# Optimization experiments

Measured on AMD Instinct MI355X. Metric: run time of the kernel, lower is better.

The kernel has to match this reference:

```python
import jax, jax.numpy as jnp
import numpy as np

DIM = 1024
NUM_HEADS = 16
HEAD_DIM = DIM // NUM_HEADS


def setup_inputs() -> dict:
    key = jax.random.key(0)
    k_x, k_q, k_k, k_v, k_o = jax.random.split(key, 5)
    B, L = 2, 2048
    scale = 1.0 / np.sqrt(DIM)
    x_bld = jax.random.normal(k_x, (B, L, DIM), dtype=jnp.float32)
    # LinearGeneral kernels: (in_features, num_heads, head_dim) for q/k/v,
    # (num_heads, head_dim, out_features) for out. Init ~ lecun_normal-ish scale.
    Wq = jax.random.normal(k_q, (DIM, NUM_HEADS, HEAD_DIM), dtype=jnp.float32) * scale
    Wk = jax.random.normal(k_k, (DIM, NUM_HEADS, HEAD_DIM), dtype=jnp.float32) * scale
    Wv = jax.random.normal(k_v, (DIM, NUM_HEADS, HEAD_DIM), dtype=jnp.float32) * scale
    Wo = jax.random.normal(k_o, (NUM_HEADS, HEAD_DIM, DIM), dtype=jnp.float32) * scale
    return {"x_bld": x_bld, "Wq": Wq, "Wk": Wk, "Wv": Wv, "Wo": Wo}


def reference(x_bld, Wq, Wk, Wv, Wo) -> jnp.ndarray:
    # Projections: [B,L,D] x [D,H,hd] -> [B,L,H,hd]
    q_blhd = jnp.einsum('bld,dhk->blhk', x_bld, Wq)
    k_blhd = jnp.einsum('bld,dhk->blhk', x_bld, Wk)
    v_blhd = jnp.einsum('bld,dhk->blhk', x_bld, Wv)
    # Scores: [B,H,L,L]
    attn_bhll = jnp.einsum('bqhd,bkhd->bhqk', q_blhd, k_blhd)
    attn_bhll = attn_bhll / jnp.sqrt(jnp.asarray(HEAD_DIM, dtype=attn_bhll.dtype))
    L = x_bld.shape[1]
    qi = jnp.arange(L)[:, None]
    ki = jnp.arange(L)[None, :]
    mask_ll = ki <= qi  # causal, no window
    neg_inf = jnp.finfo(attn_bhll.dtype).min
    attn_bhll = jnp.where(mask_ll[None, None, :, :], attn_bhll, neg_inf)
    attn_bhll = jax.nn.softmax(attn_bhll, axis=-1)
    y_blhd = jnp.einsum('bhqk,bkhd->bqhd', attn_bhll, v_blhd)
    # Output projection: contract (H, hd) -> D
    return jnp.einsum('blhk,hkd->bld', y_blhd, Wo)
```

## Files before the change

kernel.cpp:

```cpp
#include <hip/hip_runtime.h>
#include <hip/hip_bf16.h>

typedef __hip_bfloat16 bf16;
typedef __attribute__((ext_vector_type(8))) short short8;
typedef __attribute__((ext_vector_type(4))) float f32x4;

__device__ __forceinline__ float bfbits2f(unsigned short u) {
    return __uint_as_float(((unsigned int)u) << 16);
}
__device__ __forceinline__ unsigned short f2bfbits(float f) {
    union { float f; unsigned int u; } x;
    x.f = f;
    unsigned int r = x.u + 0x7FFFu + ((x.u >> 16) & 1u);
    return (unsigned short)(r >> 16);
}
__device__ __forceinline__ unsigned int pack_bf16x2(float lo, float hi) {
    unsigned int u0 = __float_as_uint(lo) + 0x8000u;
    unsigned int u1 = __float_as_uint(hi) + 0x8000u;
    return __builtin_amdgcn_perm(u1, u0, 0x07060302u);
}
__device__ __forceinline__ void async_copy16(const void* g, void* l) {
    __builtin_amdgcn_global_load_lds(
        (const __attribute__((address_space(1))) void*)g,
        (__attribute__((address_space(3))) void*)l, 16, 0, 0);
}
__device__ __forceinline__ bool sniff_bf16(const unsigned int* p, int lane) {
    unsigned int wd = p[lane];
    unsigned int e = (wd >> 7) & 0xFFu;
    return __popcll(__ballot(e >= 90u && e <= 150u)) > 40;
}

__global__ __launch_bounds__(256) void prep(
    const void* __restrict__ X, const void* __restrict__ W1,
    const void* __restrict__ W2, const void* __restrict__ W3,
    const void* __restrict__ W4, short* __restrict__ xb,
    short* __restrict__ O1, short* __restrict__ O2,
    short* __restrict__ O3, short* __restrict__ O4) {
    __shared__ float tbuf[32][33];
    const int bx = blockIdx.x;
    const int tid = threadIdx.x;
    const int lane = tid & 63;

    if (bx < 2048) {
        const bool isBf = sniff_bf16((const unsigned int*)X, lane);
        const int i = (bx * 256 + tid) * 8;
        if (isBf) {
            *(short8*)&xb[i] = *(const short8*)((const short*)X + i);
        } else {
            const float* xf = (const float*)X + i;
            float4 a = *(const float4*)xf;
            float4 b = *(const float4*)(xf + 4);
            short8 o;
            o[0] = (short)f2bfbits(a.x); o[1] = (short)f2bfbits(a.y);
            o[2] = (short)f2bfbits(a.z); o[3] = (short)f2bfbits(a.w);
            o[4] = (short)f2bfbits(b.x); o[5] = (short)f2bfbits(b.y);
            o[6] = (short)f2bfbits(b.z); o[7] = (short)f2bfbits(b.w);
            *(short8*)&xb[i] = o;
        }
    } else {
        const void* Ws[4] = {W1, W2, W3, W4};
        short* Os[4] = {O1, O2, O3, O4};
        const int t = bx - 2048;
        const int wsel = t >> 10;
        const int tile = t & 1023;
        const int bxt = tile & 31, byt = tile >> 5;
        const void* W = Ws[wsel];
        const bool isBf = sniff_bf16((const unsigned int*)W, lane);
        const float scale = (wsel == 0) ? 0.125f : 1.0f;
        short* O = Os[wsel];

        const int tx = tid & 31, ty = tid >> 5;
        const int gx = bxt * 32 + tx;
#pragma unroll
        for (int i = 0; i < 4; i++) {
            const int gy = byt * 32 + ty + i * 8;
            float v = isBf
                ? bfbits2f(((const unsigned short*)W)[(size_t)gy * 1024 + gx])
                : ((const float*)W)[(size_t)gy * 1024 + gx];
            tbuf[ty + i * 8][tx] = v * scale;
        }
        __syncthreads();
#pragma unroll
        for (int i = 0; i < 4; i++) {
            const int orow = bxt * 32 + ty + i * 8;
            const int ocol = byt * 32 + tx;
            O[(size_t)orow * 1024 + ocol] = (short)f2bfbits(tbuf[tx][ty + i * 8]);
        }
    }
}

__global__ __launch_bounds__(256) void transpose_v(const short* __restrict__ qkv,
                                                   short* __restrict__ VtG) {
    __shared__ short t[32][33];
    const int tx = threadIdx.x & 31, ty = threadIdx.x >> 5;
    const int b = blockIdx.z >> 4, h = blockIdx.z & 15;
    const int l0 = blockIdx.x * 32, d0 = blockIdx.y * 32;
#pragma unroll
    for (int i = 0; i < 4; i++) {
        const int l = l0 + ty + i * 8;
        t[ty + i * 8][tx] =
            qkv[(size_t)(b * 2048 + l) * 3072 + 2048 + h * 64 + d0 + tx];
    }
    __syncthreads();
    const int ptx = 2 * (tx & 15) + (tx >> 4);
#pragma unroll
    for (int i = 0; i < 4; i++) {
        const int d = d0 + ty + i * 8;
        VtG[((size_t)(b * 16 + h) * 64 + d) * 2048 + l0 + ptx] = t[tx][ty + i * 8];
    }
}

template <int BN>
__global__ __launch_bounds__(256) void gemm_async(const short* __restrict__ A,
                                                  const short* __restrict__ Bt,
                                                  void* __restrict__ C,
                                                  const unsigned int* __restrict__ xdet,
                                                  int M, int N, int K) {
    __shared__ short As[2][128 * 32];
    __shared__ short Bs[2][BN * 32];
    constexpr int NI = BN / 32;

    const int tid = threadIdx.x;
    const int lane = tid & 63;
    const int wv = __builtin_amdgcn_readfirstlane(tid >> 6);
    const int quad = lane >> 4, l16 = lane & 15;
    const int wr = wv >> 1, wc = wv & 1;
    const int m0 = blockIdx.y * 128, n0 = blockIdx.x * BN;

    const int gr = lane >> 2;
    const int gc = (lane & 3) * 8;

    const f32x4 zero = {0.f, 0.f, 0.f, 0.f};
    f32x4 acc[4][NI];
#pragma unroll
    for (int mi = 0; mi < 4; mi++)
#pragma unroll
        for (int ni = 0; ni < NI; ni++) acc[mi][ni] = zero;

    const short* aptr[2];
    const short* bptr[BN / 64];
#pragma unroll
    for (int t = 0; t < 2; t++)
        aptr[t] = A + (size_t)(m0 + t * 64 + wv * 16 + gr) * K + gc;
#pragma unroll
    for (int t = 0; t < BN / 64; t++)
        bptr[t] = Bt + (size_t)(n0 + t * 64 + wv * 16 + gr) * K + gc;

#pragma unroll
    for (int t = 0; t < 2; t++) async_copy16(aptr[t], &As[0][(t * 64 + wv * 16) * 32]);
#pragma unroll
    for (int t = 0; t < BN / 64; t++) async_copy16(bptr[t], &Bs[0][(t * 64 + wv * 16) * 32]);

    for (int k0 = 0; k0 < K; k0 += 32) {
        const int cur = (k0 >> 5) & 1;
        __syncthreads();
        if (k0 + 32 < K) {
            const int nxt = cur ^ 1;
#pragma unroll
            for (int t = 0; t < 2; t++)
                async_copy16(aptr[t] + k0 + 32, &As[nxt][(t * 64 + wv * 16) * 32]);
#pragma unroll
            for (int t = 0; t < BN / 64; t++)
                async_copy16(bptr[t] + k0 + 32, &Bs[nxt][(t * 64 + wv * 16) * 32]);
        }

        short8 af[4], bfv[NI];
#pragma unroll
        for (int mi = 0; mi < 4; mi++)
            af[mi] = *(const short8*)&As[cur][(wr * 64 + mi * 16 + l16) * 32 + quad * 8];
#pragma unroll
        for (int ni = 0; ni < NI; ni++)
            bfv[ni] = *(const short8*)&Bs[cur][(wc * (BN / 2) + ni * 16 + l16) * 32 + quad * 8];
#pragma unroll
        for (int mi = 0; mi < 4; mi++)
#pragma unroll
            for (int ni = 0; ni < NI; ni++)
                acc[mi][ni] = __builtin_amdgcn_mfma_f32_16x16x32_bf16(
                    af[mi], bfv[ni], acc[mi][ni], 0, 0, 0);
    }

    bool outBf = true;
    if (xdet) outBf = sniff_bf16(xdet, lane);
    if (outBf) {
        unsigned short* Cb = (unsigned short*)C;
#pragma unroll
        for (int mi = 0; mi < 4; mi++)
#pragma unroll
            for (int ni = 0; ni < NI; ni++)
#pragma unroll
                for (int r = 0; r < 4; r++) {
                    const int row = m0 + wr * 64 + mi * 16 + quad * 4 + r;
                    const int col = n0 + wc * (BN / 2) + ni * 16 + l16;
                    Cb[(size_t)row * N + col] = f2bfbits(acc[mi][ni][r]);
                }
    } else {
        float* Cf = (float*)C;
#pragma unroll
        for (int mi = 0; mi < 4; mi++)
#pragma unroll
            for (int ni = 0; ni < NI; ni++)
#pragma unroll
                for (int r = 0; r < 4; r++) {
                    const int row = m0 + wr * 64 + mi * 16 + quad * 4 + r;
                    const int col = n0 + wc * (BN / 2) + ni * 16 + l16;
                    Cf[(size_t)row * N + col] = acc[mi][ni][r];
                }
    }
}

__global__ __launch_bounds__(256) void attn_mfma6(
    const short* __restrict__ qkv, const short* __restrict__ VtG,
    short* __restrict__ Yg, short* __restrict__ Opart, float* __restrict__ ml) {
    __shared__ short Ks[2][2 * 64 * 32];
    __shared__ short Vt[2][2 * 64 * 32];
    __shared__ short Ps[2 * 64 * 32];

    const int tid = threadIdx.x;
    const int lane = tid & 63;
    const int wv = __builtin_amdgcn_readfirstlane(tid >> 6);
    const int quad = lane >> 4, l16 = lane & 15;
    const int bh = blockIdx.x;
    const int b = bh >> 4, h = bh & 15;

    int qb, seg, S;
    const int slot = blockIdx.y;
    if (slot < 64)      { qb = 31 - (slot >> 2); seg = slot & 3; S = 4; }
    else if (slot < 80) { const int t2 = slot - 64; qb = 15 - (t2 >> 1); seg = t2 & 1; S = 2; }
    else                { qb = 87 - slot; seg = 0; S = 1; }

    const int ns = qb + 1;
    const int sb0 = seg * ns / S;
    const int sb1 = (seg + 1) * ns / S;

    const int lr = lane >> 2;
    const int lc = (lane & 3) * 8;

    const short* kptr[2];
    const short* vptr[2];
    short* kdst[2];
    short* vdst[2];
#pragma unroll
    for (int i = 0; i < 2; i++) {
        const int u = wv * 2 + i;
        const int half = u & 1, g16 = (u >> 1) * 16;
        kptr[i] = qkv + (size_t)(b * 2048 + sb0 * 64 + g16 + lr) * 3072 + 1024 +
                  h * 64 + half * 32 + lc;
        kdst[i] = &Ks[0][(half * 64 + g16) * 32];
        vptr[i] = VtG + ((size_t)bh * 64 + g16 + lr) * 2048 + sb0 * 64 +
                  half * 32 + lc;
        vdst[i] = &Vt[0][(half * 64 + g16) * 32];
    }
    const int bufoff = 2 * 64 * 32;
    const int buf0 = sb0 & 1;
    const int qbuf = buf0 ^ 1;

#pragma unroll
    for (int i = 0; i < 2; i++) {
        const int u = wv * 2 + i;
        const int half = u & 1, g16 = (u >> 1) * 16;
        const short* qsrc = qkv + (size_t)(b * 2048 + qb * 64 + g16 + lr) * 3072 +
                            h * 64 + half * 32 + lc;
        async_copy16(qsrc, &Ks[qbuf][(half * 64 + g16) * 32]);
        async_copy16(kptr[i], kdst[i] + buf0 * bufoff);
        async_copy16(vptr[i], vdst[i] + buf0 * bufoff);
        kptr[i] += 64 * 3072;
        vptr[i] += 64;
    }
    __syncthreads();
    const short8 qf0 = *(const short8*)&Ks[qbuf][(wv * 16 + l16) * 32 + quad * 8];
    const short8 qf1 = *(const short8*)&Ks[qbuf][(64 + wv * 16 + l16) * 32 + quad * 8];
    __syncthreads();

    unsigned int* Psd = (unsigned int*)Ps;
    const f32x4 minit = {-12.f, -12.f, -12.f, -12.f};
    f32x4 O[4];
#pragma unroll
    for (int ni = 0; ni < 4; ni++) O[ni] = {0.f, 0.f, 0.f, 0.f};
    float l_st[4] = {0.f, 0.f, 0.f, 0.f};
    const int qrow0 = qb * 64 + wv * 16 + quad * 4;

    for (int sb = sb0; sb < sb1; sb++) {
        const int cur = sb & 1;
        if (sb != sb0) __syncthreads();
        if (sb + 1 < sb1) {
            const int nxt = cur ^ 1;
#pragma unroll
            for (int i = 0; i < 2; i++) {
                async_copy16(kptr[i], kdst[i] + nxt * bufoff);
                async_copy16(vptr[i], vdst[i] + nxt * bufoff);
                kptr[i] += 64 * 3072;
                vptr[i] += 64;
            }
        }
        const short* Kc = &Ks[cur][0];
        const short* Vc = &Vt[cur][0];

        f32x4 s[4];
#pragma unroll
        for (int ni = 0; ni < 4; ni++) {
            short8 kf0 = *(const short8*)&Kc[(ni * 16 + l16) * 32 + quad * 8];
            short8 kf1 = *(const short8*)&Kc[(64 + ni * 16 + l16) * 32 + quad * 8];
            s[ni] = __builtin_amdgcn_mfma_f32_16x16x32_bf16(qf0, kf0, minit, 0, 0, 0);
            s[ni] = __builtin_amdgcn_mfma_f32_16x16x32_bf16(qf1, kf1, s[ni], 0, 0, 0);
        }

        if (sb == qb) {
#pragma unroll
            for (int ni = 0; ni < 4; ni++) {
                const int key = sb * 64 + ni * 16 + l16;
#pragma unroll
                for (int r = 0; r < 4; r++)
                    if (key > qrow0 + r) s[ni][r] = -1e30f;
            }
        }

#pragma unroll
        for (int ni = 0; ni < 4; ni++)
#pragma unroll
            for (int r = 0; r < 4; r++) s[ni][r] = __expf(s[ni][r]);
#pragma unroll
        for (int r = 0; r < 4; r++)
            l_st[r] += (s[0][r] + s[1][r]) + (s[2][r] + s[3][r]);

#pragma unroll
        for (int c = 0; c < 2; c++)
#pragma unroll
            for (int r = 0; r < 4; r++)
                Psd[(c * 64 + wv * 16 + quad * 4 + r) * 16 + l16] =
                    pack_bf16x2(s[2 * c][r], s[2 * c + 1][r]);

        short8 pf[2];
#pragma unroll
        for (int c = 0; c < 2; c++)
            pf[c] = *(const short8*)&Ps[(c * 64 + wv * 16 + l16) * 32 + quad * 8];

#pragma unroll
        for (int ni = 0; ni < 4; ni++)
#pragma unroll
            for (int c = 0; c < 2; c++) {
                short8 vf = *(const short8*)&Vc[(c * 64 + ni * 16 + l16) * 32 + quad * 8];
                O[ni] = __builtin_amdgcn_mfma_f32_16x16x32_bf16(pf[c], vf, O[ni], 0, 0, 0);
            }
    }

    float lt[4];
#pragma unroll
    for (int r = 0; r < 4; r++) {
        float v = l_st[r];
        v += __shfl_xor(v, 1);
        v += __shfl_xor(v, 2);
        v += __shfl_xor(v, 4);
        v += __shfl_xor(v, 8);
        lt[r] = v;
    }

    if (S == 1) {
#pragma unroll
        for (int r = 0; r < 4; r++) {
            const float inv = 1.f / lt[r];
            const int qrow = qrow0 + r;
#pragma unroll
            for (int ni = 0; ni < 4; ni++)
                Yg[(size_t)(b * 2048 + qrow) * 1024 + h * 64 + ni * 16 + l16] =
                    (short)f2bfbits(O[ni][r] * inv);
        }
    } else {
        const int qidx = qb - 8;
        const int base = ((seg * 32 + bh) * 24 + qidx) * 64;
#pragma unroll
        for (int r = 0; r < 4; r++) {
            const int q = wv * 16 + quad * 4 + r;
#pragma unroll
            for (int ni = 0; ni < 4; ni++)
                Opart[(size_t)(base + q) * 64 + ni * 16 + l16] =
                    (short)f2bfbits(O[ni][r]);
            if (l16 == 0) ml[base + q] = lt[r];
        }
    }
}

__global__ __launch_bounds__(256) void attn_combine6(
    const short* __restrict__ Opart, const float* __restrict__ ml,
    short* __restrict__ Yg) {
    const int qb = 8 + blockIdx.x;
    const int bh = blockIdx.y;
    const int b = bh >> 4, h = bh & 15;
    const int S = (qb >= 16) ? 4 : 2;
    const int qidx = qb - 8;
    const int tid = threadIdx.x;
    const int q = tid >> 2;
    const int d0 = (tid & 3) * 16;

    float a0[8] = {}, a1[8] = {};
    float lsum = 0.f;
    for (int s = 0; s < S; s++) {
        const int idx = ((s * 32 + bh) * 24 + qidx) * 64 + q;
        lsum += ml[idx];
        const short* p = Opart + (size_t)idx * 64 + d0;
        short8 x0 = *(const short8*)p;
        short8 x1 = *(const short8*)(p + 8);
#pragma unroll
        for (int t = 0; t < 8; t++) {
            a0[t] += bfbits2f((unsigned short)x0[t]);
            a1[t] += bfbits2f((unsigned short)x1[t]);
        }
    }
    const float inv = 1.f / lsum;
    short8 o0, o1;
#pragma unroll
    for (int t = 0; t < 8; t++) {
        o0[t] = (short)f2bfbits(a0[t] * inv);
        o1[t] = (short)f2bfbits(a1[t] * inv);
    }
    short* yp = Yg + (size_t)(b * 2048 + qb * 64 + q) * 1024 + h * 64 + d0;
    *(short8*)yp = o0;
    *(short8*)(yp + 8) = o1;
}

extern "C" void kernel_launch(void* const* d_in, const int* in_sizes, int n_in,
                              void* d_out, int out_size, void* d_ws, size_t ws_size,
                              hipStream_t stream) {
    const int M = 2 * 2048;
    const int D = 1024;

    char* w = (char*)d_ws;
    short* xb  = (short*)w;
    short* WqT = (short*)(w + (8u << 20));
    short* WkT = WqT + (1u << 20);
    short* WvT = WkT + (1u << 20);
    short* WoT = WvT + (1u << 20);
    short* qkv = WoT + (1u << 20);
    short* VtG = qkv + (size_t)M * 3072;
    short* Opart = VtG + (size_t)2048 * 2048;
    float* mlp = (float*)(Opart + (size_t)4 * 32 * 24 * 64 * 64);
    short* y = xb;

    prep<<<6144, 256, 0, stream>>>(d_in[0], d_in[1], d_in[2], d_in[3], d_in[4],
                                   xb, WqT, WkT, WvT, WoT);

    gemm_async<128><<<dim3(3072 / 128, M / 128), 256, 0, stream>>>(
        xb, WqT, qkv, nullptr, M, 3072, D);

    transpose_v<<<dim3(64, 2, 32), 256, 0, stream>>>(qkv, VtG);

    attn_mfma6<<<dim3(32, 88), 256, 0, stream>>>(qkv, VtG, y, Opart, mlp);
    attn_combine6<<<dim3(24, 32), 256, 0, stream>>>(Opart, mlp, y);

    gemm_async<64><<<dim3(D / 64, M / 128), 256, 0, stream>>>(
        y, WoT, d_out, (const unsigned int*)d_in[0], M, D, D);
}
```

Measured before the change: 187.9 us.

## XOR-swizzle LDS layouts in GEMM and attention kernels to avoid bank conflicts

Applies XOR swizzling to the shared-memory tiles in the projection GEMM (A/B tiles) and in the attention kernel (Q/K/V tiles and the P staging buffer). The attention K/V tiles change from a split two-half 32-column layout to a full 64-column row layout, with swizzled column chunks on both the async global-to-LDS copies and the MFMA fragment reads. The goal is to remove LDS bank conflicts on the short8 fragment loads. It adds some index arithmetic, and the write and read swizzles must match exactly or the results will be wrong.

```diff
diff --git a/kernel.cpp b/kernel.cpp
--- a/kernel.cpp
+++ b/kernel.cpp
@@ -128,7 +128,7 @@
     const int m0 = blockIdx.y * 128, n0 = blockIdx.x * BN;
 
     const int gr = lane >> 2;
-    const int gc = (lane & 3) * 8;
+    const int gc = ((lane & 3) ^ ((lane >> 3) & 3)) * 8;
 
     const f32x4 zero = {0.f, 0.f, 0.f, 0.f};
     f32x4 acc[4][NI];
@@ -150,6 +150,8 @@
     for (int t = 0; t < 2; t++) async_copy16(aptr[t], &As[0][(t * 64 + wv * 16) * 32]);
 #pragma unroll
     for (int t = 0; t < BN / 64; t++) async_copy16(bptr[t], &Bs[0][(t * 64 + wv * 16) * 32]);
+
+    const int ss = (quad ^ ((l16 >> 1) & 3)) * 8;
 
     for (int k0 = 0; k0 < K; k0 += 32) {
         const int cur = (k0 >> 5) & 1;
@@ -167,10 +169,10 @@
         short8 af[4], bfv[NI];
 #pragma unroll
         for (int mi = 0; mi < 4; mi++)
-            af[mi] = *(const short8*)&As[cur][(wr * 64 + mi * 16 + l16) * 32 + quad * 8];
+            af[mi] = *(const short8*)&As[cur][(wr * 64 + mi * 16 + l16) * 32 + ss];
 #pragma unroll
         for (int ni = 0; ni < NI; ni++)
-            bfv[ni] = *(const short8*)&Bs[cur][(wc * (BN / 2) + ni * 16 + l16) * 32 + quad * 8];
+            bfv[ni] = *(const short8*)&Bs[cur][(wc * (BN / 2) + ni * 16 + l16) * 32 + ss];
 #pragma unroll
         for (int mi = 0; mi < 4; mi++)
 #pragma unroll
@@ -211,8 +213,8 @@
 __global__ __launch_bounds__(256) void attn_mfma6(
     const short* __restrict__ qkv, const short* __restrict__ VtG,
     short* __restrict__ Yg, short* __restrict__ Opart, float* __restrict__ ml) {
-    __shared__ short Ks[2][2 * 64 * 32];
-    __shared__ short Vt[2][2 * 64 * 32];
+    __shared__ short Ks[2][64 * 64];
+    __shared__ short Vt[2][64 * 64];
     __shared__ short Ps[2 * 64 * 32];
 
     const int tid = threadIdx.x;
@@ -232,8 +234,8 @@
     const int sb0 = seg * ns / S;
     const int sb1 = (seg + 1) * ns / S;
 
-    const int lr = lane >> 2;
-    const int lc = (lane & 3) * 8;
+    const int rr = lane >> 3;
+    const int scol = ((lane & 7) ^ rr) * 8;
 
     const short* kptr[2];
     const short* vptr[2];
@@ -242,33 +244,31 @@
 #pragma unroll
     for (int i = 0; i < 2; i++) {
         const int u = wv * 2 + i;
-        const int half = u & 1, g16 = (u >> 1) * 16;
-        kptr[i] = qkv + (size_t)(b * 2048 + sb0 * 64 + g16 + lr) * 3072 + 1024 +
-                  h * 64 + half * 32 + lc;
-        kdst[i] = &Ks[0][(half * 64 + g16) * 32];
-        vptr[i] = VtG + ((size_t)bh * 64 + g16 + lr) * 2048 + sb0 * 64 +
-                  half * 32 + lc;
-        vdst[i] = &Vt[0][(half * 64 + g16) * 32];
-    }
-    const int bufoff = 2 * 64 * 32;
+        kptr[i] = qkv + (size_t)(b * 2048 + sb0 * 64 + u * 8 + rr) * 3072 + 1024 +
+                  h * 64 + scol;
+        kdst[i] = &Ks[0][(u * 8) * 64];
+        vptr[i] = VtG + ((size_t)bh * 64 + u * 8 + rr) * 2048 + sb0 * 64 + scol;
+        vdst[i] = &Vt[0][(u * 8) * 64];
+    }
+    const int bufoff = 64 * 64;
     const int buf0 = sb0 & 1;
     const int qbuf = buf0 ^ 1;
 
 #pragma unroll
     for (int i = 0; i < 2; i++) {
         const int u = wv * 2 + i;
-        const int half = u & 1, g16 = (u >> 1) * 16;
-        const short* qsrc = qkv + (size_t)(b * 2048 + qb * 64 + g16 + lr) * 3072 +
-                            h * 64 + half * 32 + lc;
-        async_copy16(qsrc, &Ks[qbuf][(half * 64 + g16) * 32]);
+        const short* qsrc = qkv + (size_t)(b * 2048 + qb * 64 + u * 8 + rr) * 3072 +
+                            h * 64 + scol;
+        async_copy16(qsrc, &Ks[qbuf][(u * 8) * 64]);
         async_copy16(kptr[i], kdst[i] + buf0 * bufoff);
         async_copy16(vptr[i], vdst[i] + buf0 * bufoff);
         kptr[i] += 64 * 3072;
         vptr[i] += 64;
     }
     __syncthreads();
-    const short8 qf0 = *(const short8*)&Ks[qbuf][(wv * 16 + l16) * 32 + quad * 8];
-    const short8 qf1 = *(const short8*)&Ks[qbuf][(64 + wv * 16 + l16) * 32 + quad * 8];
+    const int sl = (quad ^ (l16 & 7)) * 8;
+    const short8 qf0 = *(const short8*)&Ks[qbuf][(wv * 16 + l16) * 64 + sl];
+    const short8 qf1 = *(const short8*)&Ks[qbuf][(wv * 16 + l16) * 64 + (sl ^ 32)];
     __syncthreads();
 
     unsigned int* Psd = (unsigned int*)Ps;
@@ -278,6 +278,7 @@
     for (int ni = 0; ni < 4; ni++) O[ni] = {0.f, 0.f, 0.f, 0.f};
     float l_st[4] = {0.f, 0.f, 0.f, 0.f};
     const int qrow0 = qb * 64 + wv * 16 + quad * 4;
+    const int psl = (quad ^ ((l16 >> 2) & 3)) * 8;
 
     for (int sb = sb0; sb < sb1; sb++) {
         const int cur = sb & 1;
@@ -298,8 +299,8 @@
         f32x4 s[4];
 #pragma unroll
         for (int ni = 0; ni < 4; ni++) {
-            short8 kf0 = *(const short8*)&Kc[(ni * 16 + l16) * 32 + quad * 8];
-            short8 kf1 = *(const short8*)&Kc[(64 + ni * 16 + l16) * 32 + quad * 8];
+            short8 kf0 = *(const short8*)&Kc[(ni * 16 + l16) * 64 + sl];
+            short8 kf1 = *(const short8*)&Kc[(ni * 16 + l16) * 64 + (sl ^ 32)];
             s[ni] = __builtin_amdgcn_mfma_f32_16x16x32_bf16(qf0, kf0, minit, 0, 0, 0);
             s[ni] = __builtin_amdgcn_mfma_f32_16x16x32_bf16(qf1, kf1, s[ni], 0, 0, 0);
         }
@@ -326,19 +327,19 @@
         for (int c = 0; c < 2; c++)
 #pragma unroll
             for (int r = 0; r < 4; r++)
-                Psd[(c * 64 + wv * 16 + quad * 4 + r) * 16 + l16] =
+                Psd[(c * 64 + wv * 16 + quad * 4 + r) * 16 + (l16 ^ (quad << 2))] =
                     pack_bf16x2(s[2 * c][r], s[2 * c + 1][r]);
 
         short8 pf[2];
 #pragma unroll
         for (int c = 0; c < 2; c++)
-            pf[c] = *(const short8*)&Ps[(c * 64 + wv * 16 + l16) * 32 + quad * 8];
+            pf[c] = *(const short8*)&Ps[(c * 64 + wv * 16 + l16) * 32 + psl];
 
 #pragma unroll
         for (int ni = 0; ni < 4; ni++)
 #pragma unroll
             for (int c = 0; c < 2; c++) {
-                short8 vf = *(const short8*)&Vc[(c * 64 + ni * 16 + l16) * 32 + quad * 8];
+                short8 vf = *(const short8*)&Vc[(ni * 16 + l16) * 64 + (sl ^ (c << 5))];
                 O[ni] = __builtin_amdgcn_mfma_f32_16x16x32_bf16(pf[c], vf, O[ni], 0, 0, 0);
             }
     }
```

Measured after the change: 184.5 us. Within noise of the previous version (-1.8%).
